# Optimization experiments

Measured on AMD Instinct MI355X. Metric: run time of the kernel, lower is better.

Reference implementation:

```python
import jax, jax.numpy as jnp
import numpy as np

B, C, HID, H, W = 32, 1024, 512, 56, 56

def setup_inputs() -> dict:
    key = jax.random.key(0)
    ks = jax.random.split(key, 8)
    s = 0.02
    return {
        "x":  jax.random.normal(ks[0], (B, C, H, W), dtype=jnp.float32),
        "W1": jax.random.normal(ks[1], (C, HID), dtype=jnp.float32) * s,  # mlp Linear(C->hidden), no bias
        "W2": jax.random.normal(ks[2], (HID, C), dtype=jnp.float32) * s,  # mlp Linear(hidden->C), no bias
        "WA": jax.random.normal(ks[3], (C, H), dtype=jnp.float32) * s,    # fc_A weight (transposed)
        "bA": jax.random.normal(ks[4], (H,), dtype=jnp.float32) * s,
        "WB": jax.random.normal(ks[5], (C, W), dtype=jnp.float32) * s,    # fc_B weight (transposed)
        "bB": jax.random.normal(ks[6], (W,), dtype=jnp.float32) * s,
    }

def reference(x, W1, W2, WA, bA, WB, bB):
    # Global average pool over spatial dims: (B, C)
    y = jnp.mean(x, axis=(2, 3))
    # MLP with exact (erf) GELU; dropout is identity in eval mode
    h = jax.nn.gelu(y @ W1, approximate=False)          # (B, HID)
    yp = jax.nn.gelu(h @ W2, approximate=False)          # (B, C)
    # Original replicates yp across C channels before fc_A/fc_B, so every
    # channel's attention map is identical: compute once, broadcast.
    A = yp @ WA + bA                                     # (B, H)
    Bv = yp @ WB + bB                                    # (B, W)
    attn = jax.nn.sigmoid(A[:, None, :, None] * Bv[:, None, None, :])  # (B, 1, H, W)
    return jnp.broadcast_to(attn, (x.shape[0], x.shape[1], A.shape[1], Bv.shape[1]))
```

## Files before the change

### kernel.cpp

```cpp
#include <hip/hip_runtime.h>
#include <math.h>

#define BATCH 32
#define NC    1024
#define NHID  512
#define NH    56
#define NW    56
#define HWSZ  3136
#define HW4   784

typedef float nfloat4 __attribute__((ext_vector_type(4)));

__device__ __forceinline__ float gelu_exact(float x) {
    return 0.5f * x * (1.0f + erff(x * 0.7071067811865476f));
}

__global__ __launch_bounds__(256) void gap_kernel(const float* __restrict__ x,
                                                  float* __restrict__ y) {
    const int row  = (blockIdx.x << 2) | (threadIdx.x >> 6);
    const int lane = threadIdx.x & 63;
    const nfloat4* xr = (const nfloat4*)(x + (size_t)row * HWSZ);

    float s = 0.f;
#pragma unroll
    for (int it = 0; it < 12; ++it) {
        nfloat4 v = __builtin_nontemporal_load(xr + lane + (it << 6));
        s += (v.x + v.y) + (v.z + v.w);
    }
    if (lane < 16) {
        nfloat4 v = __builtin_nontemporal_load(xr + 768 + lane);
        s += (v.x + v.y) + (v.z + v.w);
    }
#pragma unroll
    for (int off = 32; off > 0; off >>= 1) s += __shfl_down(s, off);
    if (lane == 0) y[row] = s * (1.0f / 3136.0f);
}

__global__ __launch_bounds__(256) void fc1_kernel(const float* __restrict__ y,
                                                  const float* __restrict__ W1,
                                                  float* __restrict__ h) {
    const int jc = blockIdx.x;
    const int b  = blockIdx.y;
    const int t  = threadIdx.x;

    __shared__ float sy[NC];
    __shared__ nfloat4 part[256];
    for (int i = t; i < NC; i += 256) sy[i] = y[b * NC + i];
    __syncthreads();

    const int lane4 = t & 15;
    const int j0 = jc * 64 + lane4 * 4;
    const int ks = (t >> 4) * 64;

    nfloat4 acc0 = {0.f, 0.f, 0.f, 0.f};
    nfloat4 acc1 = {0.f, 0.f, 0.f, 0.f};
    const float* wbase = W1 + (size_t)ks * NHID + j0;
#pragma unroll 8
    for (int c = 0; c < 64; c += 2) {
        nfloat4 w0 = *(const nfloat4*)(wbase + (size_t)(c + 0) * NHID);
        nfloat4 w1 = *(const nfloat4*)(wbase + (size_t)(c + 1) * NHID);
        acc0 += sy[ks + c + 0] * w0;
        acc1 += sy[ks + c + 1] * w1;
    }
    part[t] = acc0 + acc1;
    __syncthreads();
    if (t < 16) {
        nfloat4 s = part[t];
#pragma unroll
        for (int g = 1; g < 16; ++g) s += part[g * 16 + t];
        float* hp = h + b * NHID + jc * 64 + t * 4;
        hp[0] = gelu_exact(s.x);
        hp[1] = gelu_exact(s.y);
        hp[2] = gelu_exact(s.z);
        hp[3] = gelu_exact(s.w);
    }
}

__global__ __launch_bounds__(256) void fc2_kernel(const float* __restrict__ h,
                                                  const float* __restrict__ W2,
                                                  float* __restrict__ yp) {
    const int cc = blockIdx.x;
    const int b  = blockIdx.y;
    const int t  = threadIdx.x;

    __shared__ float sh[NHID];
    __shared__ nfloat4 part[256];
    for (int i = t; i < NHID; i += 256) sh[i] = h[b * NHID + i];
    __syncthreads();

    const int lane4 = t & 15;
    const int c0 = cc * 64 + lane4 * 4;
    const int js = (t >> 4) * 32;

    nfloat4 acc0 = {0.f, 0.f, 0.f, 0.f};
    nfloat4 acc1 = {0.f, 0.f, 0.f, 0.f};
    const float* wbase = W2 + (size_t)js * NC + c0;
#pragma unroll 8
    for (int jj = 0; jj < 32; jj += 2) {
        nfloat4 w0 = *(const nfloat4*)(wbase + (size_t)(jj + 0) * NC);
        nfloat4 w1 = *(const nfloat4*)(wbase + (size_t)(jj + 1) * NC);
        acc0 += sh[js + jj + 0] * w0;
        acc1 += sh[js + jj + 1] * w1;
    }
    part[t] = acc0 + acc1;
    __syncthreads();
    if (t < 16) {
        nfloat4 s = part[t];
#pragma unroll
        for (int g = 1; g < 16; ++g) s += part[g * 16 + t];
        float* pp = yp + b * NC + cc * 64 + t * 4;
        pp[0] = gelu_exact(s.x);
        pp[1] = gelu_exact(s.y);
        pp[2] = gelu_exact(s.z);
        pp[3] = gelu_exact(s.w);
    }
}

__global__ __launch_bounds__(512) void ab_kernel(
    const float* __restrict__ yp, const float* __restrict__ WA,
    const float* __restrict__ bA, const float* __restrict__ WB,
    const float* __restrict__ bB, float* __restrict__ AB) {
    const int b = blockIdx.x;
    const int t = threadIdx.x;

    __shared__ float sp[NC];
    __shared__ float partA[512];
    __shared__ float partB[512];
    for (int i = t; i < NC; i += 512) sp[i] = yp[b * NC + i];
    __syncthreads();

    const int i  = t & 63;
    const int ks = (t >> 6) * 128;
    float a0 = 0.f, a1 = 0.f, a2 = 0.f, a3 = 0.f;
    float b0 = 0.f, b1 = 0.f, b2 = 0.f, b3 = 0.f;
    if (i < NH) {
        const float* wa = WA + (size_t)ks * NH + i;
        const float* wb = WB + (size_t)ks * NW + i;
        for (int c = 0; c < 128; c += 4) {
            a0 += sp[ks + c + 0] * wa[(size_t)(c + 0) * NH];
            a1 += sp[ks + c + 1] * wa[(size_t)(c + 1) * NH];
            a2 += sp[ks + c + 2] * wa[(size_t)(c + 2) * NH];
            a3 += sp[ks + c + 3] * wa[(size_t)(c + 3) * NH];
            b0 += sp[ks + c + 0] * wb[(size_t)(c + 0) * NW];
            b1 += sp[ks + c + 1] * wb[(size_t)(c + 1) * NW];
            b2 += sp[ks + c + 2] * wb[(size_t)(c + 2) * NW];
            b3 += sp[ks + c + 3] * wb[(size_t)(c + 3) * NW];
        }
    }
    partA[t] = (a0 + a1) + (a2 + a3);
    partB[t] = (b0 + b1) + (b2 + b3);
    __syncthreads();
    if (t < NH) {
        float sa = bA[t], sb = bB[t];
#pragma unroll
        for (int g = 0; g < 8; ++g) {
            sa += partA[g * 64 + t];
            sb += partB[g * 64 + t];
        }
        AB[b * 128 + t] = sa;
        AB[b * 128 + 64 + t] = sb;
    }
}

__global__ __launch_bounds__(256) void bcast_kernel(const float* __restrict__ AB,
                                                    float* __restrict__ out) {
    const int blk = blockIdx.x;
    const int b = blk >> 6;
    const int cchunk = blk & 63;
    const int t = threadIdx.x;

    __shared__ float sA[NH];
    __shared__ float sB[NW];
    if (t < NH) sA[t] = AB[b * 128 + t];
    else if (t >= 64 && t < 64 + NW) sB[t - 64] = AB[b * 128 + t];
    __syncthreads();

    nfloat4 v[4];
#pragma unroll
    for (int it = 0; it < 4; ++it) {
        const int idx = t + it * 256;
        if (idx < HW4) {
            const int r  = idx / 14;
            const int cb = (idx - r * 14) * 4;
            const float a = sA[r];
            nfloat4 q;
            q.x = 1.0f / (1.0f + expf(-(a * sB[cb + 0])));
            q.y = 1.0f / (1.0f + expf(-(a * sB[cb + 1])));
            q.z = 1.0f / (1.0f + expf(-(a * sB[cb + 2])));
            q.w = 1.0f / (1.0f + expf(-(a * sB[cb + 3])));
            v[it] = q;
        }
    }

    const size_t base = ((size_t)b * NC + (size_t)cchunk * 16) * HW4;
#pragma unroll
    for (int ch = 0; ch < 16; ++ch) {
        nfloat4* orow = (nfloat4*)out + base + (size_t)ch * HW4;
#pragma unroll
        for (int it = 0; it < 4; ++it) {
            const int idx = t + it * 256;
            if (idx < HW4) __builtin_nontemporal_store(v[it], &orow[idx]);
        }
    }
}

extern "C" void kernel_launch(void* const* d_in, const int* in_sizes, int n_in,
                              void* d_out, int out_size, void* d_ws, size_t ws_size,
                              hipStream_t stream) {
    const float* x  = (const float*)d_in[0];
    const float* W1 = (const float*)d_in[1];
    const float* W2 = (const float*)d_in[2];
    const float* WA = (const float*)d_in[3];
    const float* bA = (const float*)d_in[4];
    const float* WB = (const float*)d_in[5];
    const float* bB = (const float*)d_in[6];
    float* out = (float*)d_out;

    float* y  = (float*)d_ws;
    float* yp = y;
    float* h  = y + BATCH * NC;
    float* AB = h + BATCH * NHID;

    gap_kernel<<<BATCH * NC / 4, 256, 0, stream>>>(x, y);
    fc1_kernel<<<dim3(NHID / 64, BATCH), 256, 0, stream>>>(y, W1, h);
    fc2_kernel<<<dim3(NC / 64, BATCH), 256, 0, stream>>>(h, W2, yp);
    ab_kernel<<<BATCH, 512, 0, stream>>>(yp, WA, bA, WB, bB, AB);
    bcast_kernel<<<BATCH * (NC / 16), 256, 0, stream>>>(AB, out);
}
```

Baseline: 162.5 us.

## Fuse fc1, fc2 and fc_A/fc_B into one per-batch MLP kernel

Replaces the three small kernels (fc1, fc2, ab) with a single 1024-thread kernel per batch element that keeps the hidden and projected vectors in shared memory. This removes two kernel launches and the global round-trips of h and yp. In exchange, only 32 blocks run, so each block streams all of W1 and W2 by itself (8 MB total weight reads across batches versus previously spread over many more blocks), which may reduce parallelism for the GEMV stages.

```diff
diff --git a/kernel.cpp b/kernel.cpp
--- a/kernel.cpp
+++ b/kernel.cpp
@@ -36,124 +36,107 @@
     if (lane == 0) y[row] = s * (1.0f / 3136.0f);
 }
 
-__global__ __launch_bounds__(256) void fc1_kernel(const float* __restrict__ y,
-                                                  const float* __restrict__ W1,
-                                                  float* __restrict__ h) {
-    const int jc = blockIdx.x;
-    const int b  = blockIdx.y;
-    const int t  = threadIdx.x;
-
-    __shared__ float sy[NC];
-    __shared__ nfloat4 part[256];
-    for (int i = t; i < NC; i += 256) sy[i] = y[b * NC + i];
-    __syncthreads();
-
-    const int lane4 = t & 15;
-    const int j0 = jc * 64 + lane4 * 4;
-    const int ks = (t >> 4) * 64;
-
-    nfloat4 acc0 = {0.f, 0.f, 0.f, 0.f};
-    nfloat4 acc1 = {0.f, 0.f, 0.f, 0.f};
-    const float* wbase = W1 + (size_t)ks * NHID + j0;
-#pragma unroll 8
-    for (int c = 0; c < 64; c += 2) {
-        nfloat4 w0 = *(const nfloat4*)(wbase + (size_t)(c + 0) * NHID);
-        nfloat4 w1 = *(const nfloat4*)(wbase + (size_t)(c + 1) * NHID);
-        acc0 += sy[ks + c + 0] * w0;
-        acc1 += sy[ks + c + 1] * w1;
-    }
-    part[t] = acc0 + acc1;
-    __syncthreads();
-    if (t < 16) {
-        nfloat4 s = part[t];
-#pragma unroll
-        for (int g = 1; g < 16; ++g) s += part[g * 16 + t];
-        float* hp = h + b * NHID + jc * 64 + t * 4;
-        hp[0] = gelu_exact(s.x);
-        hp[1] = gelu_exact(s.y);
-        hp[2] = gelu_exact(s.z);
-        hp[3] = gelu_exact(s.w);
-    }
-}
-
-__global__ __launch_bounds__(256) void fc2_kernel(const float* __restrict__ h,
-                                                  const float* __restrict__ W2,
-                                                  float* __restrict__ yp) {
-    const int cc = blockIdx.x;
-    const int b  = blockIdx.y;
-    const int t  = threadIdx.x;
-
-    __shared__ float sh[NHID];
-    __shared__ nfloat4 part[256];
-    for (int i = t; i < NHID; i += 256) sh[i] = h[b * NHID + i];
-    __syncthreads();
-
-    const int lane4 = t & 15;
-    const int c0 = cc * 64 + lane4 * 4;
-    const int js = (t >> 4) * 32;
-
-    nfloat4 acc0 = {0.f, 0.f, 0.f, 0.f};
-    nfloat4 acc1 = {0.f, 0.f, 0.f, 0.f};
-    const float* wbase = W2 + (size_t)js * NC + c0;
-#pragma unroll 8
-    for (int jj = 0; jj < 32; jj += 2) {
-        nfloat4 w0 = *(const nfloat4*)(wbase + (size_t)(jj + 0) * NC);
-        nfloat4 w1 = *(const nfloat4*)(wbase + (size_t)(jj + 1) * NC);
-        acc0 += sh[js + jj + 0] * w0;
-        acc1 += sh[js + jj + 1] * w1;
-    }
-    part[t] = acc0 + acc1;
-    __syncthreads();
-    if (t < 16) {
-        nfloat4 s = part[t];
-#pragma unroll
-        for (int g = 1; g < 16; ++g) s += part[g * 16 + t];
-        float* pp = yp + b * NC + cc * 64 + t * 4;
-        pp[0] = gelu_exact(s.x);
-        pp[1] = gelu_exact(s.y);
-        pp[2] = gelu_exact(s.z);
-        pp[3] = gelu_exact(s.w);
-    }
-}
-
-__global__ __launch_bounds__(512) void ab_kernel(
-    const float* __restrict__ yp, const float* __restrict__ WA,
+__global__ __launch_bounds__(1024) void mlp_kernel(
+    const float* __restrict__ y,  const float* __restrict__ W1,
+    const float* __restrict__ W2, const float* __restrict__ WA,
     const float* __restrict__ bA, const float* __restrict__ WB,
     const float* __restrict__ bB, float* __restrict__ AB) {
     const int b = blockIdx.x;
     const int t = threadIdx.x;
 
-    __shared__ float sp[NC];
-    __shared__ float partA[512];
-    __shared__ float partB[512];
-    for (int i = t; i < NC; i += 512) sp[i] = yp[b * NC + i];
-    __syncthreads();
-
-    const int i  = t & 63;
-    const int ks = (t >> 6) * 128;
-    float a0 = 0.f, a1 = 0.f, a2 = 0.f, a3 = 0.f;
-    float b0 = 0.f, b1 = 0.f, b2 = 0.f, b3 = 0.f;
-    if (i < NH) {
-        const float* wa = WA + (size_t)ks * NH + i;
-        const float* wb = WB + (size_t)ks * NW + i;
-        for (int c = 0; c < 128; c += 4) {
-            a0 += sp[ks + c + 0] * wa[(size_t)(c + 0) * NH];
-            a1 += sp[ks + c + 1] * wa[(size_t)(c + 1) * NH];
-            a2 += sp[ks + c + 2] * wa[(size_t)(c + 2) * NH];
-            a3 += sp[ks + c + 3] * wa[(size_t)(c + 3) * NH];
-            b0 += sp[ks + c + 0] * wb[(size_t)(c + 0) * NW];
-            b1 += sp[ks + c + 1] * wb[(size_t)(c + 1) * NW];
-            b2 += sp[ks + c + 2] * wb[(size_t)(c + 2) * NW];
-            b3 += sp[ks + c + 3] * wb[(size_t)(c + 3) * NW];
-        }
-    }
-    partA[t] = (a0 + a1) + (a2 + a3);
-    partB[t] = (b0 + b1) + (b2 + b3);
+    __shared__ float   sy[NC];
+    __shared__ float   sh[NHID];
+    __shared__ float   syp[NC];
+    __shared__ nfloat4 part[1024];
+    __shared__ float   partA[1024];
+    __shared__ float   partB[1024];
+
+    sy[t] = y[b * NC + t];
+    __syncthreads();
+
+    {
+        const int lane = t & 127;
+        const int j0   = lane * 4;
+        const int ks   = (t >> 7) * 128;
+        nfloat4 acc0 = {0.f, 0.f, 0.f, 0.f};
+        nfloat4 acc1 = {0.f, 0.f, 0.f, 0.f};
+        const float* wp = W1 + (size_t)ks * NHID + j0;
+#pragma unroll 4
+        for (int c = 0; c < 128; c += 2) {
+            nfloat4 w0 = *(const nfloat4*)(wp + (size_t)(c + 0) * NHID);
+            nfloat4 w1 = *(const nfloat4*)(wp + (size_t)(c + 1) * NHID);
+            acc0 += sy[ks + c + 0] * w0;
+            acc1 += sy[ks + c + 1] * w1;
+        }
+        part[t] = acc0 + acc1;
+    }
+    __syncthreads();
+    if (t < 128) {
+        nfloat4 s = part[t];
+#pragma unroll
+        for (int g = 1; g < 8; ++g) s += part[g * 128 + t];
+        sh[t * 4 + 0] = gelu_exact(s.x);
+        sh[t * 4 + 1] = gelu_exact(s.y);
+        sh[t * 4 + 2] = gelu_exact(s.z);
+        sh[t * 4 + 3] = gelu_exact(s.w);
+    }
+    __syncthreads();
+
+    {
+        const int lane = t & 255;
+        const int c0   = lane * 4;
+        const int js   = (t >> 8) * 128;
+        nfloat4 acc0 = {0.f, 0.f, 0.f, 0.f};
+        nfloat4 acc1 = {0.f, 0.f, 0.f, 0.f};
+        const float* wp = W2 + (size_t)js * NC + c0;
+#pragma unroll 4
+        for (int jj = 0; jj < 128; jj += 2) {
+            nfloat4 w0 = *(const nfloat4*)(wp + (size_t)(jj + 0) * NC);
+            nfloat4 w1 = *(const nfloat4*)(wp + (size_t)(jj + 1) * NC);
+            acc0 += sh[js + jj + 0] * w0;
+            acc1 += sh[js + jj + 1] * w1;
+        }
+        part[t] = acc0 + acc1;
+    }
+    __syncthreads();
+    if (t < 256) {
+        nfloat4 s = part[t];
+#pragma unroll
+        for (int g = 1; g < 4; ++g) s += part[g * 256 + t];
+        syp[t * 4 + 0] = gelu_exact(s.x);
+        syp[t * 4 + 1] = gelu_exact(s.y);
+        syp[t * 4 + 2] = gelu_exact(s.z);
+        syp[t * 4 + 3] = gelu_exact(s.w);
+    }
+    __syncthreads();
+
+    {
+        const int i  = t & 63;
+        const int ks = (t >> 6) * 64;
+        float a0 = 0.f, a1 = 0.f, a2 = 0.f, a3 = 0.f;
+        float b0 = 0.f, b1 = 0.f, b2 = 0.f, b3 = 0.f;
+        if (i < NH) {
+            const float* wa = WA + (size_t)ks * NH + i;
+            const float* wb = WB + (size_t)ks * NW + i;
+            for (int c = 0; c < 64; c += 4) {
+                a0 += syp[ks + c + 0] * wa[(size_t)(c + 0) * NH];
+                a1 += syp[ks + c + 1] * wa[(size_t)(c + 1) * NH];
+                a2 += syp[ks + c + 2] * wa[(size_t)(c + 2) * NH];
+                a3 += syp[ks + c + 3] * wa[(size_t)(c + 3) * NH];
+                b0 += syp[ks + c + 0] * wb[(size_t)(c + 0) * NW];
+                b1 += syp[ks + c + 1] * wb[(size_t)(c + 1) * NW];
+                b2 += syp[ks + c + 2] * wb[(size_t)(c + 2) * NW];
+                b3 += syp[ks + c + 3] * wb[(size_t)(c + 3) * NW];
+            }
+        }
+        partA[t] = (a0 + a1) + (a2 + a3);
+        partB[t] = (b0 + b1) + (b2 + b3);
+    }
     __syncthreads();
     if (t < NH) {
         float sa = bA[t], sb = bB[t];
 #pragma unroll
-        for (int g = 0; g < 8; ++g) {
+        for (int g = 0; g < 16; ++g) {
             sa += partA[g * 64 + t];
             sb += partB[g * 64 + t];
         }
@@ -217,13 +200,9 @@
     float* out = (float*)d_out;
 
     float* y  = (float*)d_ws;
-    float* yp = y;
-    float* h  = y + BATCH * NC;
-    float* AB = h + BATCH * NHID;
+    float* AB = y + BATCH * NC;
 
     gap_kernel<<<BATCH * NC / 4, 256, 0, stream>>>(x, y);
-    fc1_kernel<<<dim3(NHID / 64, BATCH), 256, 0, stream>>>(y, W1, h);
-    fc2_kernel<<<dim3(NC / 64, BATCH), 256, 0, stream>>>(h, W2, yp);
-    ab_kernel<<<BATCH, 512, 0, stream>>>(yp, WA, bA, WB, bB, AB);
+    mlp_kernel<<<BATCH, 1024, 0, stream>>>(y, W1, W2, WA, bA, WB, bB, AB);
     bcast_kernel<<<BATCH * (NC / 16), 256, 0, stream>>>(AB, out);
 }
```

Measured after the change: 191.4 us. +17.8%, slower.

## Prefetch MLP weights into L2 during GAP tail and widen FC grids

Applied to the files above, without the earlier changes.

The last 1152 blocks of the pooling kernel now also load W1, W2, WA and WB, so those weights are warm in L2 (or MALL) when the small GEMV kernels run. fc1 and fc2 now give each block 32 output columns instead of 64, doubling the grid for more parallelism, and use a two-stage shared-memory reduction. ab_kernel switches to float4 loads over a 16-lane layout. The aim is to cut the latency-bound weight fetches in the serial MLP chain, at the cost of extra memory traffic in the bandwidth-bound pooling pass.

```diff
diff --git a/kernel.cpp b/kernel.cpp
--- a/kernel.cpp
+++ b/kernel.cpp
@@ -16,7 +16,11 @@
 }
 
 __global__ __launch_bounds__(256) void gap_kernel(const float* __restrict__ x,
-                                                  float* __restrict__ y) {
+                                                  float* __restrict__ y,
+                                                  const float* __restrict__ W1,
+                                                  const float* __restrict__ W2,
+                                                  const float* __restrict__ WA,
+                                                  const float* __restrict__ WB) {
     const int row  = (blockIdx.x << 2) | (threadIdx.x >> 6);
     const int lane = threadIdx.x & 63;
     const nfloat4* xr = (const nfloat4*)(x + (size_t)row * HWSZ);
@@ -34,6 +38,29 @@
 #pragma unroll
     for (int off = 32; off > 0; off >>= 1) s += __shfl_down(s, off);
     if (lane == 0) y[row] = s * (1.0f / 3136.0f);
+
+    const int pb = (int)blockIdx.x - (BATCH * NC / 4 - 1152);
+    if (pb >= 0) {
+        const int t = threadIdx.x;
+        float sink = 0.f;
+        if (pb < 512) {
+            nfloat4 w = ((const nfloat4*)W1)[pb * 256 + t];
+            sink = w.x + w.w;
+        } else if (pb < 1024) {
+            nfloat4 w = ((const nfloat4*)W2)[(pb - 512) * 256 + t];
+            sink = w.x + w.w;
+        } else {
+            const int q = pb - 1024;
+            if (q < 56) {
+                nfloat4 w = ((const nfloat4*)WA)[q * 256 + t];
+                sink = w.x;
+            } else if (q < 112) {
+                nfloat4 w = ((const nfloat4*)WB)[(q - 56) * 256 + t];
+                sink = w.x;
+            }
+        }
+        asm volatile("" :: "v"(sink));
+    }
 }
 
 __global__ __launch_bounds__(256) void fc1_kernel(const float* __restrict__ y,
@@ -43,20 +70,21 @@
     const int b  = blockIdx.y;
     const int t  = threadIdx.x;
 
-    __shared__ float sy[NC];
+    __shared__ float   sy[NC];
     __shared__ nfloat4 part[256];
+    __shared__ nfloat4 spart[64];
     for (int i = t; i < NC; i += 256) sy[i] = y[b * NC + i];
     __syncthreads();
 
-    const int lane4 = t & 15;
-    const int j0 = jc * 64 + lane4 * 4;
-    const int ks = (t >> 4) * 64;
+    const int lane8 = t & 7;
+    const int j0 = jc * 32 + lane8 * 4;
+    const int ks = (t >> 3) * 32;
 
     nfloat4 acc0 = {0.f, 0.f, 0.f, 0.f};
     nfloat4 acc1 = {0.f, 0.f, 0.f, 0.f};
     const float* wbase = W1 + (size_t)ks * NHID + j0;
 #pragma unroll 8
-    for (int c = 0; c < 64; c += 2) {
+    for (int c = 0; c < 32; c += 2) {
         nfloat4 w0 = *(const nfloat4*)(wbase + (size_t)(c + 0) * NHID);
         nfloat4 w1 = *(const nfloat4*)(wbase + (size_t)(c + 1) * NHID);
         acc0 += sy[ks + c + 0] * w0;
@@ -64,11 +92,13 @@
     }
     part[t] = acc0 + acc1;
     __syncthreads();
-    if (t < 16) {
-        nfloat4 s = part[t];
-#pragma unroll
-        for (int g = 1; g < 16; ++g) s += part[g * 16 + t];
-        float* hp = h + b * NHID + jc * 64 + t * 4;
+    if (t < 64) spart[t] = part[t] + part[t + 64] + part[t + 128] + part[t + 192];
+    __syncthreads();
+    if (t < 8) {
+        nfloat4 s = spart[t];
+#pragma unroll
+        for (int g = 1; g < 8; ++g) s += spart[g * 8 + t];
+        float* hp = h + b * NHID + jc * 32 + t * 4;
         hp[0] = gelu_exact(s.x);
         hp[1] = gelu_exact(s.y);
         hp[2] = gelu_exact(s.z);
@@ -83,20 +113,21 @@
     const int b  = blockIdx.y;
     const int t  = threadIdx.x;
 
-    __shared__ float sh[NHID];
+    __shared__ float   sh[NHID];
     __shared__ nfloat4 part[256];
+    __shared__ nfloat4 spart[64];
     for (int i = t; i < NHID; i += 256) sh[i] = h[b * NHID + i];
     __syncthreads();
 
-    const int lane4 = t & 15;
-    const int c0 = cc * 64 + lane4 * 4;
-    const int js = (t >> 4) * 32;
+    const int lane8 = t & 7;
+    const int c0 = cc * 32 + lane8 * 4;
+    const int js = (t >> 3) * 16;
 
     nfloat4 acc0 = {0.f, 0.f, 0.f, 0.f};
     nfloat4 acc1 = {0.f, 0.f, 0.f, 0.f};
     const float* wbase = W2 + (size_t)js * NC + c0;
 #pragma unroll 8
-    for (int jj = 0; jj < 32; jj += 2) {
+    for (int jj = 0; jj < 16; jj += 2) {
         nfloat4 w0 = *(const nfloat4*)(wbase + (size_t)(jj + 0) * NC);
         nfloat4 w1 = *(const nfloat4*)(wbase + (size_t)(jj + 1) * NC);
         acc0 += sh[js + jj + 0] * w0;
@@ -104,11 +135,13 @@
     }
     part[t] = acc0 + acc1;
     __syncthreads();
-    if (t < 16) {
-        nfloat4 s = part[t];
-#pragma unroll
-        for (int g = 1; g < 16; ++g) s += part[g * 16 + t];
-        float* pp = yp + b * NC + cc * 64 + t * 4;
+    if (t < 64) spart[t] = part[t] + part[t + 64] + part[t + 128] + part[t + 192];
+    __syncthreads();
+    if (t < 8) {
+        nfloat4 s = spart[t];
+#pragma unroll
+        for (int g = 1; g < 8; ++g) s += spart[g * 8 + t];
+        float* pp = yp + b * NC + cc * 32 + t * 4;
         pp[0] = gelu_exact(s.x);
         pp[1] = gelu_exact(s.y);
         pp[2] = gelu_exact(s.z);
@@ -123,42 +156,53 @@
     const int b = blockIdx.x;
     const int t = threadIdx.x;
 
-    __shared__ float sp[NC];
-    __shared__ float partA[512];
-    __shared__ float partB[512];
+    __shared__ float   sp[NC];
+    __shared__ nfloat4 partA[512];
+    __shared__ nfloat4 partB[512];
     for (int i = t; i < NC; i += 512) sp[i] = yp[b * NC + i];
     __syncthreads();
 
-    const int i  = t & 63;
-    const int ks = (t >> 6) * 128;
-    float a0 = 0.f, a1 = 0.f, a2 = 0.f, a3 = 0.f;
-    float b0 = 0.f, b1 = 0.f, b2 = 0.f, b3 = 0.f;
-    if (i < NH) {
-        const float* wa = WA + (size_t)ks * NH + i;
-        const float* wb = WB + (size_t)ks * NW + i;
-        for (int c = 0; c < 128; c += 4) {
-            a0 += sp[ks + c + 0] * wa[(size_t)(c + 0) * NH];
-            a1 += sp[ks + c + 1] * wa[(size_t)(c + 1) * NH];
-            a2 += sp[ks + c + 2] * wa[(size_t)(c + 2) * NH];
-            a3 += sp[ks + c + 3] * wa[(size_t)(c + 3) * NH];
-            b0 += sp[ks + c + 0] * wb[(size_t)(c + 0) * NW];
-            b1 += sp[ks + c + 1] * wb[(size_t)(c + 1) * NW];
-            b2 += sp[ks + c + 2] * wb[(size_t)(c + 2) * NW];
-            b3 += sp[ks + c + 3] * wb[(size_t)(c + 3) * NW];
-        }
-    }
-    partA[t] = (a0 + a1) + (a2 + a3);
-    partB[t] = (b0 + b1) + (b2 + b3);
-    __syncthreads();
-    if (t < NH) {
-        float sa = bA[t], sb = bB[t];
-#pragma unroll
-        for (int g = 0; g < 8; ++g) {
-            sa += partA[g * 64 + t];
-            sb += partB[g * 64 + t];
-        }
-        AB[b * 128 + t] = sa;
-        AB[b * 128 + 64 + t] = sb;
+    const int grp    = t >> 4;
+    const int lane16 = t & 15;
+    const int ks     = grp * 32;
+    nfloat4 accA = {0.f, 0.f, 0.f, 0.f};
+    nfloat4 accB = {0.f, 0.f, 0.f, 0.f};
+    if (lane16 < 14) {
+        const nfloat4* wa = (const nfloat4*)WA + (size_t)ks * 14 + lane16;
+        const nfloat4* wb = (const nfloat4*)WB + (size_t)ks * 14 + lane16;
+#pragma unroll 8
+        for (int c = 0; c < 32; ++c) {
+            const float sv = sp[ks + c];
+            accA += sv * wa[(size_t)c * 14];
+            accB += sv * wb[(size_t)c * 14];
+        }
+    }
+    partA[t] = accA;
+    partB[t] = accB;
+    __syncthreads();
+    if (t < 16) {
+        nfloat4 s = partA[t];
+#pragma unroll
+        for (int g = 1; g < 32; ++g) s += partA[g * 16 + t];
+        if (t < 14) {
+            const int i0 = t * 4;
+            AB[b * 128 + i0 + 0] = bA[i0 + 0] + s.x;
+            AB[b * 128 + i0 + 1] = bA[i0 + 1] + s.y;
+            AB[b * 128 + i0 + 2] = bA[i0 + 2] + s.z;
+            AB[b * 128 + i0 + 3] = bA[i0 + 3] + s.w;
+        }
+    } else if (t < 32) {
+        const int l = t - 16;
+        nfloat4 s = partB[l];
+#pragma unroll
+        for (int g = 1; g < 32; ++g) s += partB[g * 16 + l];
+        if (l < 14) {
+            const int i0 = l * 4;
+            AB[b * 128 + 64 + i0 + 0] = bB[i0 + 0] + s.x;
+            AB[b * 128 + 64 + i0 + 1] = bB[i0 + 1] + s.y;
+            AB[b * 128 + 64 + i0 + 2] = bB[i0 + 2] + s.z;
+            AB[b * 128 + 64 + i0 + 3] = bB[i0 + 3] + s.w;
+        }
     }
 }
 
@@ -221,9 +265,9 @@
     float* h  = y + BATCH * NC;
     float* AB = h + BATCH * NHID;
 
-    gap_kernel<<<BATCH * NC / 4, 256, 0, stream>>>(x, y);
-    fc1_kernel<<<dim3(NHID / 64, BATCH), 256, 0, stream>>>(y, W1, h);
-    fc2_kernel<<<dim3(NC / 64, BATCH), 256, 0, stream>>>(h, W2, yp);
+    gap_kernel<<<BATCH * NC / 4, 256, 0, stream>>>(x, y, W1, W2, WA, WB);
+    fc1_kernel<<<dim3(NHID / 32, BATCH), 256, 0, stream>>>(y, W1, h);
+    fc2_kernel<<<dim3(NC / 32, BATCH), 256, 0, stream>>>(h, W2, yp);
     ab_kernel<<<BATCH, 512, 0, stream>>>(yp, WA, bA, WB, bB, AB);
     bcast_kernel<<<BATCH * (NC / 16), 256, 0, stream>>>(AB, out);
 }
```

Result: no change. 163.6 us (+0.6%).
